# Kernel optimization log

Measured on AMD Instinct MI355X. Metric: run time of the kernel, lower is better.

## Reference

```python
import jax, jax.numpy as jnp
import numpy as np
from jax import lax

B, D, H = 16384, 64, 1024
CLAMP = 10.0


def _masks(D, H):
    # Exactly mirrors MADE.create_masks (numpy, static).
    m_in = np.arange(D)
    m0 = np.arange(H) % (D - 1)
    mask1 = (m_in[None, :] <= m0[:, None]).astype(np.float32)        # [H, D]
    base = (m0[None, :] < m_in[:, None]).astype(np.float32)          # [D, H]
    mask2 = np.repeat(base, 2, axis=0).astype(np.float32)            # [2D, H] (rows interleaved, as np.repeat)
    return jnp.asarray(mask1), jnp.asarray(mask2)


def setup_inputs() -> dict:
    key = jax.random.key(0)
    k1, k2, k3 = jax.random.split(key, 3)
    z = jax.random.normal(k1, (B, D), dtype=jnp.float32)
    xavier_std = 0.01 * np.sqrt(2.0 / (D + H))  # xavier_normal_ with gain=0.01
    W1 = jax.random.normal(k2, (H, D), dtype=jnp.float32) * xavier_std
    b1 = jnp.zeros((H,), dtype=jnp.float32)
    # original zero-inits W2 (degenerate identity flow); use small random instead
    W2 = jax.random.normal(k3, (2 * D, H), dtype=jnp.float32) * 0.01
    b2 = jnp.zeros((2 * D,), dtype=jnp.float32)
    return {"z": z, "W1": W1, "b1": b1, "W2": W2, "b2": b2}


def reference(z, W1, b1, W2, b2):
    Bd, Dd = z.shape
    Hd = W1.shape[0]
    mask1, mask2 = _masks(Dd, Hd)
    W1m = W1 * mask1
    W2m = W2 * mask2

    def conditioner(x):  # MADE.forward
        h = jnp.tanh(x @ W1m.T + b1)                 # [B, H]
        return jnp.clip(h @ W2m.T + b2, -CLAMP, CLAMP)  # [B, 2D]

    def step(carry, i):
        x, ld = carry
        params = conditioner(x)
        mu = params[:, :Dd]
        alpha = jnp.clip(params[:, Dd:], -CLAMP, CLAMP)
        a_i = alpha[:, i]                            # [B]
        x_i = z[:, i] * jnp.exp(a_i) + mu[:, i]
        x = x.at[:, i].set(x_i)
        return (x, ld + a_i), None

    init = (jnp.zeros_like(z), jnp.zeros((Bd,), dtype=z.dtype))
    (x, log_det), _ = lax.scan(step, init, jnp.arange(Dd))

    x = jnp.where(jnp.isnan(x) | jnp.isinf(x), 0.0, x)
    log_det = jnp.where(jnp.isnan(log_det) | jnp.isinf(log_det), 0.0, log_det)
    return x, log_det


if __name__ == "__main__":
    out = reference(**setup_inputs())
    print(out[0].shape, out[1].shape)
```

## Files before the change

kernel.cpp:

```cpp
#include <hip/hip_runtime.h>
#include <math.h>

#define B_DIM 16384
#define D_DIM 64
#define H_DIM 1024
#define CLAMP_V 10.0f

typedef __fp16 h2 __attribute__((ext_vector_type(2)));

__device__ __forceinline__ void inv_perm(int hp, int &c, int &h) {
    int q;
    if (hp < 272) { c = hp / 17; q = hp % 17; }
    else          { c = ((hp - 272) >> 4) + 16; q = (hp - 272) & 15; }
    h = (D_DIM - 1) * q + c;
}

__global__ __launch_bounds__(256) void maf_prep_kernel(
    const float* __restrict__ W1, const float* __restrict__ W2,
    const float* __restrict__ b1,
    __fp16* __restrict__ W1h, __fp16* __restrict__ W2h,
    __fp16* __restrict__ b1p) {
    __shared__ float smem[4224];
    __fp16* smh = reinterpret_cast<__fp16*>(smem);
    const int tid = threadIdx.x;
    const int blk = blockIdx.x;

    if (blk < 8) {
        const int hp0 = blk * 128;
        const int col = tid & 63;
        const int rr_base = tid >> 6;
        for (int rr0 = 0; rr0 < 128; rr0 += 4) {
            int rr = rr0 + rr_base;
            int c, h;
            inv_perm(hp0 + rr, c, h);
            smh[rr * 66 + col] = (__fp16)W1[h * D_DIM + col];
        }
        __syncthreads();
        const int hpt = tid & 127;
        const int ib = tid >> 7;
        int c, h;
        inv_perm(hp0 + hpt, c, h);
        for (int i0 = 0; i0 < 64; i0 += 2) {
            int i = i0 + ib;
            W1h[i * H_DIM + hp0 + hpt] =
                (i <= c) ? smh[hpt * 66 + i] : (__fp16)0.0f;
        }
    } else if (blk < 136) {
        const int j = blk - 8;
        reinterpret_cast<float4*>(smem)[tid] =
            reinterpret_cast<const float4*>(W2 + j * H_DIM)[tid];
        __syncthreads();
        const int jm = j >> 1;
#pragma unroll
        for (int kk = 0; kk < 4; kk++) {
            int hp = tid + 256 * kk;
            int c, h;
            inv_perm(hp, c, h);
            W2h[j * H_DIM + hp] = (c < jm) ? (__fp16)smem[h] : (__fp16)0.0f;
        }
    } else {
        reinterpret_cast<float4*>(smem)[tid] =
            reinterpret_cast<const float4*>(b1)[tid];
        __syncthreads();
#pragma unroll
        for (int kk = 0; kk < 4; kk++) {
            int hp = tid + 256 * kk;
            int c, h;
            inv_perm(hp, c, h);
            b1p[hp] = (__fp16)smem[h];
        }
    }
}

__device__ __forceinline__ h2 tanh_h2(h2 x) {
    h2 x2 = x * x;
    h2 p = __builtin_elementwise_fma(
        x2, h2{(__fp16)-0.33333333f, (__fp16)-0.33333333f},
        h2{(__fp16)1.0f, (__fp16)1.0f});
    return x * p;
}

__device__ __forceinline__ float clampv(float v) {
    return fminf(fmaxf(v, -CLAMP_V), CLAMP_V);
}
__device__ __forceinline__ h2 pkfma(h2 a, h2 b, h2 c) {
    return __builtin_elementwise_fma(a, b, c);
}
__device__ __forceinline__ float readlane_f(float v, int l) {
    return __int_as_float(__builtin_amdgcn_readlane(__float_as_int(v), l));
}

template<int CTRL>
__device__ __forceinline__ float dpp_add_(float v) {
    int m = __builtin_amdgcn_update_dpp(0, __float_as_int(v), CTRL, 0xf, 0xf, true);
    return v + __int_as_float(m);
}
__device__ __forceinline__ float rowsum16(float v) {
    v = dpp_add_<0x121>(v);
    v = dpp_add_<0x122>(v);
    v = dpp_add_<0x124>(v);
    v = dpp_add_<0x128>(v);
    return v;
}

__device__ __forceinline__ int stage_dst(int f) {
    int st = f / 320;
    int w  = f - st * 320;
    int base, rw;
    if (w < 64)       { base = 0;   rw = w; }
    else if (w < 192) { base = 64;  rw = w - 64; }
    else              { base = 192; rw = w - 192; }
    int c = rw >> 5, ww = rw & 31;
    return st * 320 + base + c * 32 + (ww >> 1) + ((ww & 1) << 4);
}

__device__ __forceinline__ float4 stage_ld1(int f, int gi,
        const __fp16* __restrict__ W1h, const __fp16* __restrict__ W2h) {
    int st = f / 320;
    int w  = f - st * 320;
    int i  = gi * 4 + st;
    const float4* p;
    if (w < 64)
        p = reinterpret_cast<const float4*>(W2h + i * H_DIM) + w;
    else if (w < 192)
        p = reinterpret_cast<const float4*>(W2h + (D_DIM + i) * H_DIM) + (w - 64);
    else
        p = reinterpret_cast<const float4*>(W1h + i * H_DIM) + (w - 192);
    return *p;
}

__device__ __forceinline__ void stage_load(float4 (&R)[5], int tid, int gi,
        const __fp16* __restrict__ W1h, const __fp16* __restrict__ W2h) {
#pragma unroll
    for (int kk = 0; kk < 5; kk++)
        R[kk] = stage_ld1(tid + 256 * kk, gi, W1h, W2h);
}

__device__ __forceinline__ void stage_write(float4* slabF4, float4 (&R)[5],
                                            int tid) {
#pragma unroll
    for (int kk = 0; kk < 5; kk++)
        slabF4[stage_dst(tid + 256 * kk)] = R[kk];
}

template<int MU, int AL, int UL>
__device__ __forceinline__ void lds_loadbufs(
    const float4* __restrict__ sf4, int sb, int r,
    float4 (&wm)[2 * MU], float4 (&wa)[2 * AL], float4 (&w1)[2 * (4 - UL)])
{
#pragma unroll
    for (int k = 0; k < MU; k++) {
        wm[2 * k]     = sf4[sb + k * 32 + r];
        wm[2 * k + 1] = sf4[sb + k * 32 + r + 16];
    }
#pragma unroll
    for (int k = 0; k < AL; k++) {
        wa[2 * k]     = sf4[sb + 64 + k * 32 + r];
        wa[2 * k + 1] = sf4[sb + 64 + k * 32 + r + 16];
    }
#pragma unroll
    for (int k = 0; k < 4 - UL; k++) {
        w1[2 * k]     = sf4[sb + 192 + (UL + k) * 32 + r];
        w1[2 * k + 1] = sf4[sb + 192 + (UL + k) * 32 + r + 16];
    }
}

template<int MU, int AL, int UL, int S>
__device__ __forceinline__ void do_step(
    int i, int r, const float4* __restrict__ sf4,
    float4 (&wmC)[2 * MU], float4 (&waC)[2 * AL], float4 (&w1C)[2 * (4 - UL)],
    float4 (&wmN)[2 * MU], float4 (&waN)[2 * AL], float4 (&w1N)[2 * (4 - UL)],
    float zC0, float &zN0,
    h2 (&s)[4][8], float4 &xr, float &ld,
    const float* __restrict__ zrow0,
    float b2m_v, float b2a_v)
{
    if constexpr (S < 3) {
        lds_loadbufs<MU, AL, UL>(sf4, (S + 1) * 320, r, wmN, waN, w1N);
        zN0 = zrow0[(i + 1) & 63];
    }

    const float b2mu = readlane_f(b2m_v, i);
    const float b2al = readlane_f(b2a_v, i);

    const h2 z0 = h2{(__fp16)0.0f, (__fp16)0.0f};
    h2 aM0 = z0, aM1 = z0;
    h2 aA0 = z0, aA1 = z0, aA2 = z0, aA3 = z0;
#pragma unroll
    for (int k = 0; k < AL; k++) {
        const float* wmf = reinterpret_cast<const float*>(&wmC[2 * k]);
        const float* waf = reinterpret_cast<const float*>(&waC[2 * k]);
#pragma unroll
        for (int j = 0; j < 8; j++) {
            h2 p = (k < UL) ? s[k][j] : tanh_h2(s[k][j]);
            if (k < MU) {
                if (j & 1) aM1 = pkfma(p, __builtin_bit_cast(h2, wmf[j]), aM1);
                else       aM0 = pkfma(p, __builtin_bit_cast(h2, wmf[j]), aM0);
            }
            switch (j & 3) {
                case 0: aA0 = pkfma(p, __builtin_bit_cast(h2, waf[j]), aA0); break;
                case 1: aA1 = pkfma(p, __builtin_bit_cast(h2, waf[j]), aA1); break;
                case 2: aA2 = pkfma(p, __builtin_bit_cast(h2, waf[j]), aA2); break;
                case 3: aA3 = pkfma(p, __builtin_bit_cast(h2, waf[j]), aA3); break;
            }
        }
    }
    h2 aM = aM0 + aM1;
    h2 aA = (aA0 + aA1) + (aA2 + aA3);
    float dm = rowsum16((float)aM.x + (float)aM.y);
    float da = rowsum16((float)aA.x + (float)aA.y);

    const bool mine = (r == (i >> 2));
    float mu = clampv(dm + b2mu);
    float al = clampv(da + b2al);
    float xi = fmaf(zC0, __expf(al), mu);
    ld += al;
    if (S == 0) xr.x = mine ? xi : xr.x;
    if (S == 1) xr.y = mine ? xi : xr.y;
    if (S == 2) xr.z = mine ? xi : xr.z;
    if (S == 3) xr.w = mine ? xi : xr.w;
    __fp16 xh = (__fp16)xi;
    h2 xi2 = h2{xh, xh};
#pragma unroll
    for (int k = UL; k < 4; k++) {
        const float* w1f = reinterpret_cast<const float*>(&w1C[2 * (k - UL)]);
#pragma unroll
        for (int j = 0; j < 8; j++)
            s[k][j] = pkfma(xi2, __builtin_bit_cast(h2, w1f[j]), s[k][j]);
    }
}

template<int MU, int AL, int UL, int BUF>
__device__ __forceinline__ void do_group(
    int gi, int r, int tid,
    float4 (&slab)[2][1280], float4 (&R)[5],
    h2 (&s)[4][8], float4 &xr, float &ld,
    const float* __restrict__ zrow0, float b2m_v, float b2a_v,
    const __fp16* __restrict__ W1h, const __fp16* __restrict__ W2h)
{
    stage_write(&slab[BUF][0], R, tid);
    __syncthreads();
    stage_load(R, tid, (gi + 1) & 15, W1h, W2h);
    const float4* sf4 = &slab[BUF][0];
    float4 wmA[2 * MU], waA[2 * AL], w1A[2 * (4 - UL)];
    float4 wmB[2 * MU], waB[2 * AL], w1B[2 * (4 - UL)];
    lds_loadbufs<MU, AL, UL>(sf4, 0, r, wmA, waA, w1A);
    const int i0 = gi * 4;
    float zA0 = zrow0[i0], zB0;
    do_step<MU, AL, UL, 0>(i0,     r, sf4, wmA, waA, w1A, wmB, waB, w1B,
                           zA0, zB0, s, xr, ld, zrow0, b2m_v, b2a_v);
    do_step<MU, AL, UL, 1>(i0 + 1, r, sf4, wmB, waB, w1B, wmA, waA, w1A,
                           zB0, zA0, s, xr, ld, zrow0, b2m_v, b2a_v);
    do_step<MU, AL, UL, 2>(i0 + 2, r, sf4, wmA, waA, w1A, wmB, waB, w1B,
                           zA0, zB0, s, xr, ld, zrow0, b2m_v, b2a_v);
    do_step<MU, AL, UL, 3>(i0 + 3, r, sf4, wmB, waB, w1B, wmA, waA, w1A,
                           zB0, zA0, s, xr, ld, zrow0, b2m_v, b2a_v);
}

template<int MU, int AL, int UL>
__device__ __forceinline__ void run_phase(
    int P, int r, int tid,
    float4 (&slab)[2][1280], float4 (&R)[5],
    h2 (&s)[4][8], float4 &xr, float &ld,
    const float* __restrict__ zrow0, float b2m_v, float b2a_v,
    const __fp16* __restrict__ W1h, const __fp16* __restrict__ W2h)
{
#pragma unroll 1
    for (int pp = 0; pp < 2; pp++) {
        do_group<MU, AL, UL, 0>(4 * P + 2 * pp,     r, tid, slab, R, s, xr, ld,
                                zrow0, b2m_v, b2a_v, W1h, W2h);
        do_group<MU, AL, UL, 1>(4 * P + 2 * pp + 1, r, tid, slab, R, s, xr, ld,
                                zrow0, b2m_v, b2a_v, W1h, W2h);
    }
}

__global__ __launch_bounds__(256, 1) void maf_main_kernel(
    const float* __restrict__ z, const float* __restrict__ b2,
    const __fp16* __restrict__ W1h, const __fp16* __restrict__ W2h,
    const __fp16* __restrict__ b1p, float* __restrict__ out)
{
    __shared__ float4 slab[2][1280];
    const int tid = threadIdx.x;
    const int wave = tid >> 6;
    const int lane = tid & 63;
    const int g = lane >> 4;
    const int r = lane & 15;
    const int b0 = (blockIdx.x * 4 + wave) * 4 + g;

    h2 s[4][8];
    const h2* b1p2 = reinterpret_cast<const h2*>(b1p);
#pragma unroll
    for (int c = 0; c < 4; c++) {
        int base = c * 128 + r * 8;
#pragma unroll
        for (int j = 0; j < 8; j++) s[c][j] = b1p2[base + j];
    }

    const float* zrow0 = z + b0 * D_DIM;
    const float b2m_v = b2[lane];
    const float b2a_v = b2[D_DIM + lane];
    float4 xr = float4{0, 0, 0, 0};
    float ld = 0.0f;

    float4 R[5];
    stage_load(R, tid, 0, W1h, W2h);

    run_phase<1, 3, 0>(0, r, tid, slab, R, s, xr, ld, zrow0, b2m_v, b2a_v, W1h, W2h);
#pragma unroll
    for (int j = 0; j < 8; j++) s[0][j] = tanh_h2(s[0][j]);
    run_phase<1, 3, 1>(1, r, tid, slab, R, s, xr, ld, zrow0, b2m_v, b2a_v, W1h, W2h);
#pragma unroll
    for (int j = 0; j < 8; j++) s[1][j] = tanh_h2(s[1][j]);
    run_phase<2, 4, 2>(2, r, tid, slab, R, s, xr, ld, zrow0, b2m_v, b2a_v, W1h, W2h);
#pragma unroll
    for (int j = 0; j < 8; j++) s[2][j] = tanh_h2(s[2][j]);
    run_phase<2, 4, 3>(3, r, tid, slab, R, s, xr, ld, zrow0, b2m_v, b2a_v, W1h, W2h);

    float4 v = xr;
    v.x = isfinite(v.x) ? v.x : 0.0f;
    v.y = isfinite(v.y) ? v.y : 0.0f;
    v.z = isfinite(v.z) ? v.z : 0.0f;
    v.w = isfinite(v.w) ? v.w : 0.0f;
    *reinterpret_cast<float4*>(out + b0 * D_DIM + r * 4) = v;
    if (r == 0) {
        float l = isfinite(ld) ? ld : 0.0f;
        out[B_DIM * D_DIM + b0] = l;
    }
}

extern "C" void kernel_launch(void* const* d_in, const int* in_sizes, int n_in,
                              void* d_out, int out_size, void* d_ws, size_t ws_size,
                              hipStream_t stream) {
    const float* z  = (const float*)d_in[0];
    const float* W1 = (const float*)d_in[1];
    const float* b1 = (const float*)d_in[2];
    const float* W2 = (const float*)d_in[3];
    const float* b2 = (const float*)d_in[4];
    float* out = (float*)d_out;

    __fp16* W1h = (__fp16*)d_ws;
    __fp16* W2h = W1h + D_DIM * H_DIM;
    __fp16* b1p = W2h + 2 * D_DIM * H_DIM;

    maf_prep_kernel<<<137, 256, 0, stream>>>(W1, W2, b1, W1h, W2h, b1p);

    maf_main_kernel<<<B_DIM / 16, 256, 0, stream>>>(z, b2, W1h, W2h, b1p, out);
}
```

Baseline: 165.7 us.

## Process two batch rows per lane group to reuse LDS weight loads

Each 16-lane group now carries hidden state for two batch rows instead of one, so every weight fragment read from LDS is used twice. Blocks shrink to 128 threads (2 waves), each still covering 16 rows, and the staging loop issues 10 loads per thread instead of 5. The aim is to halve LDS weight traffic per row and cut the number of block-level barriers per row. In exchange, register pressure roughly doubles for the hidden state, and with fewer waves per block there is less latency hiding.

After: 192.6 us. 1.16x slower.

```diff
diff --git a/kernel.cpp b/kernel.cpp
--- a/kernel.cpp
+++ b/kernel.cpp
@@ -129,18 +129,18 @@
     return *p;
 }
 
-__device__ __forceinline__ void stage_load(float4 (&R)[5], int tid, int gi,
+__device__ __forceinline__ void stage_load(float4 (&R)[10], int tid, int gi,
         const __fp16* __restrict__ W1h, const __fp16* __restrict__ W2h) {
 #pragma unroll
-    for (int kk = 0; kk < 5; kk++)
-        R[kk] = stage_ld1(tid + 256 * kk, gi, W1h, W2h);
-}
-
-__device__ __forceinline__ void stage_write(float4* slabF4, float4 (&R)[5],
+    for (int kk = 0; kk < 10; kk++)
+        R[kk] = stage_ld1(tid + 128 * kk, gi, W1h, W2h);
+}
+
+__device__ __forceinline__ void stage_write(float4* slabF4, float4 (&R)[10],
                                             int tid) {
 #pragma unroll
-    for (int kk = 0; kk < 5; kk++)
-        slabF4[stage_dst(tid + 256 * kk)] = R[kk];
+    for (int kk = 0; kk < 10; kk++)
+        slabF4[stage_dst(tid + 128 * kk)] = R[kk];
 }
 
 template<int MU, int AL, int UL>
@@ -170,72 +170,82 @@
     int i, int r, const float4* __restrict__ sf4,
     float4 (&wmC)[2 * MU], float4 (&waC)[2 * AL], float4 (&w1C)[2 * (4 - UL)],
     float4 (&wmN)[2 * MU], float4 (&waN)[2 * AL], float4 (&w1N)[2 * (4 - UL)],
-    float zC0, float &zN0,
-    h2 (&s)[4][8], float4 &xr, float &ld,
-    const float* __restrict__ zrow0,
+    float zC0, float zC1, float &zN0, float &zN1,
+    h2 (&s)[2][4][8], float4 (&xr)[2], float (&ld)[2],
+    const float* __restrict__ zrow0, const float* __restrict__ zrow1,
     float b2m_v, float b2a_v)
 {
     if constexpr (S < 3) {
         lds_loadbufs<MU, AL, UL>(sf4, (S + 1) * 320, r, wmN, waN, w1N);
         zN0 = zrow0[(i + 1) & 63];
+        zN1 = zrow1[(i + 1) & 63];
     }
 
     const float b2mu = readlane_f(b2m_v, i);
     const float b2al = readlane_f(b2a_v, i);
 
-    const h2 z0 = h2{(__fp16)0.0f, (__fp16)0.0f};
-    h2 aM0 = z0, aM1 = z0;
-    h2 aA0 = z0, aA1 = z0, aA2 = z0, aA3 = z0;
-#pragma unroll
-    for (int k = 0; k < AL; k++) {
-        const float* wmf = reinterpret_cast<const float*>(&wmC[2 * k]);
-        const float* waf = reinterpret_cast<const float*>(&waC[2 * k]);
-#pragma unroll
-        for (int j = 0; j < 8; j++) {
-            h2 p = (k < UL) ? s[k][j] : tanh_h2(s[k][j]);
-            if (k < MU) {
-                if (j & 1) aM1 = pkfma(p, __builtin_bit_cast(h2, wmf[j]), aM1);
-                else       aM0 = pkfma(p, __builtin_bit_cast(h2, wmf[j]), aM0);
+    float dm[2], da[2];
+#pragma unroll
+    for (int e = 0; e < 2; e++) {
+        const h2 z0 = h2{(__fp16)0.0f, (__fp16)0.0f};
+        h2 aM0 = z0, aM1 = z0;
+        h2 aA0 = z0, aA1 = z0, aA2 = z0, aA3 = z0;
+#pragma unroll
+        for (int k = 0; k < AL; k++) {
+            const float* wmf = reinterpret_cast<const float*>(&wmC[2 * k]);
+            const float* waf = reinterpret_cast<const float*>(&waC[2 * k]);
+#pragma unroll
+            for (int j = 0; j < 8; j++) {
+                h2 p = (k < UL) ? s[e][k][j] : tanh_h2(s[e][k][j]);
+                if (k < MU) {
+                    if (j & 1) aM1 = pkfma(p, __builtin_bit_cast(h2, wmf[j]), aM1);
+                    else       aM0 = pkfma(p, __builtin_bit_cast(h2, wmf[j]), aM0);
+                }
+                switch (j & 3) {
+                    case 0: aA0 = pkfma(p, __builtin_bit_cast(h2, waf[j]), aA0); break;
+                    case 1: aA1 = pkfma(p, __builtin_bit_cast(h2, waf[j]), aA1); break;
+                    case 2: aA2 = pkfma(p, __builtin_bit_cast(h2, waf[j]), aA2); break;
+                    case 3: aA3 = pkfma(p, __builtin_bit_cast(h2, waf[j]), aA3); break;
+                }
             }
-            switch (j & 3) {
-                case 0: aA0 = pkfma(p, __builtin_bit_cast(h2, waf[j]), aA0); break;
-                case 1: aA1 = pkfma(p, __builtin_bit_cast(h2, waf[j]), aA1); break;
-                case 2: aA2 = pkfma(p, __builtin_bit_cast(h2, waf[j]), aA2); break;
-                case 3: aA3 = pkfma(p, __builtin_bit_cast(h2, waf[j]), aA3); break;
-            }
-        }
-    }
-    h2 aM = aM0 + aM1;
-    h2 aA = (aA0 + aA1) + (aA2 + aA3);
-    float dm = rowsum16((float)aM.x + (float)aM.y);
-    float da = rowsum16((float)aA.x + (float)aA.y);
+        }
+        h2 aM = aM0 + aM1;
+        h2 aA = (aA0 + aA1) + (aA2 + aA3);
+        dm[e] = rowsum16((float)aM.x + (float)aM.y);
+        da[e] = rowsum16((float)aA.x + (float)aA.y);
+    }
 
     const bool mine = (r == (i >> 2));
-    float mu = clampv(dm + b2mu);
-    float al = clampv(da + b2al);
-    float xi = fmaf(zC0, __expf(al), mu);
-    ld += al;
-    if (S == 0) xr.x = mine ? xi : xr.x;
-    if (S == 1) xr.y = mine ? xi : xr.y;
-    if (S == 2) xr.z = mine ? xi : xr.z;
-    if (S == 3) xr.w = mine ? xi : xr.w;
-    __fp16 xh = (__fp16)xi;
-    h2 xi2 = h2{xh, xh};
-#pragma unroll
-    for (int k = UL; k < 4; k++) {
-        const float* w1f = reinterpret_cast<const float*>(&w1C[2 * (k - UL)]);
-#pragma unroll
-        for (int j = 0; j < 8; j++)
-            s[k][j] = pkfma(xi2, __builtin_bit_cast(h2, w1f[j]), s[k][j]);
+#pragma unroll
+    for (int e = 0; e < 2; e++) {
+        float mu = clampv(dm[e] + b2mu);
+        float al = clampv(da[e] + b2al);
+        float zi = (e == 0) ? zC0 : zC1;
+        float xi = fmaf(zi, __expf(al), mu);
+        ld[e] += al;
+        if (S == 0) xr[e].x = mine ? xi : xr[e].x;
+        if (S == 1) xr[e].y = mine ? xi : xr[e].y;
+        if (S == 2) xr[e].z = mine ? xi : xr[e].z;
+        if (S == 3) xr[e].w = mine ? xi : xr[e].w;
+        __fp16 xh = (__fp16)xi;
+        h2 xi2 = h2{xh, xh};
+#pragma unroll
+        for (int k = UL; k < 4; k++) {
+            const float* w1f = reinterpret_cast<const float*>(&w1C[2 * (k - UL)]);
+#pragma unroll
+            for (int j = 0; j < 8; j++)
+                s[e][k][j] = pkfma(xi2, __builtin_bit_cast(h2, w1f[j]), s[e][k][j]);
+        }
     }
 }
 
 template<int MU, int AL, int UL, int BUF>
 __device__ __forceinline__ void do_group(
     int gi, int r, int tid,
-    float4 (&slab)[2][1280], float4 (&R)[5],
-    h2 (&s)[4][8], float4 &xr, float &ld,
-    const float* __restrict__ zrow0, float b2m_v, float b2a_v,
+    float4 (&slab)[2][1280], float4 (&R)[10],
+    h2 (&s)[2][4][8], float4 (&xr)[2], float (&ld)[2],
+    const float* __restrict__ zrow0, const float* __restrict__ zrow1,
+    float b2m_v, float b2a_v,
     const __fp16* __restrict__ W1h, const __fp16* __restrict__ W2h)
 {
     stage_write(&slab[BUF][0], R, tid);
@@ -246,35 +256,40 @@
     float4 wmB[2 * MU], waB[2 * AL], w1B[2 * (4 - UL)];
     lds_loadbufs<MU, AL, UL>(sf4, 0, r, wmA, waA, w1A);
     const int i0 = gi * 4;
-    float zA0 = zrow0[i0], zB0;
+    float zA0 = zrow0[i0], zA1 = zrow1[i0], zB0, zB1;
     do_step<MU, AL, UL, 0>(i0,     r, sf4, wmA, waA, w1A, wmB, waB, w1B,
-                           zA0, zB0, s, xr, ld, zrow0, b2m_v, b2a_v);
+                           zA0, zA1, zB0, zB1, s, xr, ld,
+                           zrow0, zrow1, b2m_v, b2a_v);
     do_step<MU, AL, UL, 1>(i0 + 1, r, sf4, wmB, waB, w1B, wmA, waA, w1A,
-                           zB0, zA0, s, xr, ld, zrow0, b2m_v, b2a_v);
+                           zB0, zB1, zA0, zA1, s, xr, ld,
+                           zrow0, zrow1, b2m_v, b2a_v);
     do_step<MU, AL, UL, 2>(i0 + 2, r, sf4, wmA, waA, w1A, wmB, waB, w1B,
-                           zA0, zB0, s, xr, ld, zrow0, b2m_v, b2a_v);
+                           zA0, zA1, zB0, zB1, s, xr, ld,
+                           zrow0, zrow1, b2m_v, b2a_v);
     do_step<MU, AL, UL, 3>(i0 + 3, r, sf4, wmB, waB, w1B, wmA, waA, w1A,
-                           zB0, zA0, s, xr, ld, zrow0, b2m_v, b2a_v);
+                           zB0, zB1, zA0, zA1, s, xr, ld,
+                           zrow0, zrow1, b2m_v, b2a_v);
 }
 
 template<int MU, int AL, int UL>
 __device__ __forceinline__ void run_phase(
     int P, int r, int tid,
-    float4 (&slab)[2][1280], float4 (&R)[5],
-    h2 (&s)[4][8], float4 &xr, float &ld,
-    const float* __restrict__ zrow0, float b2m_v, float b2a_v,
+    float4 (&slab)[2][1280], float4 (&R)[10],
+    h2 (&s)[2][4][8], float4 (&xr)[2], float (&ld)[2],
+    const float* __restrict__ zrow0, const float* __restrict__ zrow1,
+    float b2m_v, float b2a_v,
     const __fp16* __restrict__ W1h, const __fp16* __restrict__ W2h)
 {
 #pragma unroll 1
     for (int pp = 0; pp < 2; pp++) {
         do_group<MU, AL, UL, 0>(4 * P + 2 * pp,     r, tid, slab, R, s, xr, ld,
-                                zrow0, b2m_v, b2a_v, W1h, W2h);
+                                zrow0, zrow1, b2m_v, b2a_v, W1h, W2h);
         do_group<MU, AL, UL, 1>(4 * P + 2 * pp + 1, r, tid, slab, R, s, xr, ld,
-                                zrow0, b2m_v, b2a_v, W1h, W2h);
-    }
-}
-
-__global__ __launch_bounds__(256, 1) void maf_main_kernel(
+                                zrow0, zrow1, b2m_v, b2a_v, W1h, W2h);
+    }
+}
+
+__global__ __launch_bounds__(128, 1) void maf_main_kernel(
     const float* __restrict__ z, const float* __restrict__ b2,
     const __fp16* __restrict__ W1h, const __fp16* __restrict__ W2h,
     const __fp16* __restrict__ b1p, float* __restrict__ out)
@@ -285,46 +300,67 @@
     const int lane = tid & 63;
     const int g = lane >> 4;
     const int r = lane & 15;
-    const int b0 = (blockIdx.x * 4 + wave) * 4 + g;
-
-    h2 s[4][8];
+    const int bw = (blockIdx.x * 2 + wave) * 8;
+    const int b0 = bw + g;
+    const int b1i = bw + 4 + g;
+
+    h2 s[2][4][8];
     const h2* b1p2 = reinterpret_cast<const h2*>(b1p);
 #pragma unroll
     for (int c = 0; c < 4; c++) {
         int base = c * 128 + r * 8;
 #pragma unroll
-        for (int j = 0; j < 8; j++) s[c][j] = b1p2[base + j];
+        for (int j = 0; j < 8; j++) {
+            h2 v = b1p2[base + j];
+            s[0][c][j] = v;
+            s[1][c][j] = v;
+        }
     }
 
     const float* zrow0 = z + b0 * D_DIM;
+    const float* zrow1 = z + b1i * D_DIM;
     const float b2m_v = b2[lane];
     const float b2a_v = b2[D_DIM + lane];
-    float4 xr = float4{0, 0, 0, 0};
-    float ld = 0.0f;
-
-    float4 R[5];
+    float4 xr[2] = {float4{0, 0, 0, 0}, float4{0, 0, 0, 0}};
+    float ld[2] = {0.0f, 0.0f};
+
+    float4 R[10];
     stage_load(R, tid, 0, W1h, W2h);
 
-    run_phase<1, 3, 0>(0, r, tid, slab, R, s, xr, ld, zrow0, b2m_v, b2a_v, W1h, W2h);
-#pragma unroll
-    for (int j = 0; j < 8; j++) s[0][j] = tanh_h2(s[0][j]);
-    run_phase<1, 3, 1>(1, r, tid, slab, R, s, xr, ld, zrow0, b2m_v, b2a_v, W1h, W2h);
-#pragma unroll
-    for (int j = 0; j < 8; j++) s[1][j] = tanh_h2(s[1][j]);
-    run_phase<2, 4, 2>(2, r, tid, slab, R, s, xr, ld, zrow0, b2m_v, b2a_v, W1h, W2h);
-#pragma unroll
-    for (int j = 0; j < 8; j++) s[2][j] = tanh_h2(s[2][j]);
-    run_phase<2, 4, 3>(3, r, tid, slab, R, s, xr, ld, zrow0, b2m_v, b2a_v, W1h, W2h);
-
-    float4 v = xr;
-    v.x = isfinite(v.x) ? v.x : 0.0f;
-    v.y = isfinite(v.y) ? v.y : 0.0f;
-    v.z = isfinite(v.z) ? v.z : 0.0f;
-    v.w = isfinite(v.w) ? v.w : 0.0f;
-    *reinterpret_cast<float4*>(out + b0 * D_DIM + r * 4) = v;
-    if (r == 0) {
-        float l = isfinite(ld) ? ld : 0.0f;
-        out[B_DIM * D_DIM + b0] = l;
+    run_phase<1, 3, 0>(0, r, tid, slab, R, s, xr, ld, zrow0, zrow1,
+                       b2m_v, b2a_v, W1h, W2h);
+#pragma unroll
+    for (int e = 0; e < 2; e++)
+#pragma unroll
+        for (int j = 0; j < 8; j++) s[e][0][j] = tanh_h2(s[e][0][j]);
+    run_phase<1, 3, 1>(1, r, tid, slab, R, s, xr, ld, zrow0, zrow1,
+                       b2m_v, b2a_v, W1h, W2h);
+#pragma unroll
+    for (int e = 0; e < 2; e++)
+#pragma unroll
+        for (int j = 0; j < 8; j++) s[e][1][j] = tanh_h2(s[e][1][j]);
+    run_phase<2, 4, 2>(2, r, tid, slab, R, s, xr, ld, zrow0, zrow1,
+                       b2m_v, b2a_v, W1h, W2h);
+#pragma unroll
+    for (int e = 0; e < 2; e++)
+#pragma unroll
+        for (int j = 0; j < 8; j++) s[e][2][j] = tanh_h2(s[e][2][j]);
+    run_phase<2, 4, 3>(3, r, tid, slab, R, s, xr, ld, zrow0, zrow1,
+                       b2m_v, b2a_v, W1h, W2h);
+
+#pragma unroll
+    for (int e = 0; e < 2; e++) {
+        float4 v = xr[e];
+        v.x = isfinite(v.x) ? v.x : 0.0f;
+        v.y = isfinite(v.y) ? v.y : 0.0f;
+        v.z = isfinite(v.z) ? v.z : 0.0f;
+        v.w = isfinite(v.w) ? v.w : 0.0f;
+        int b = (e == 0) ? b0 : b1i;
+        *reinterpret_cast<float4*>(out + b * D_DIM + r * 4) = v;
+        if (r == 0) {
+            float l = isfinite(ld[e]) ? ld[e] : 0.0f;
+            out[B_DIM * D_DIM + b] = l;
+        }
     }
 }
 
@@ -344,5 +380,5 @@
 
     maf_prep_kernel<<<137, 256, 0, stream>>>(W1, W2, b1, W1h, W2h, b1p);
 
-    maf_main_kernel<<<B_DIM / 16, 256, 0, stream>>>(z, b2, W1h, W2h, b1p, out);
-}
+    maf_main_kernel<<<B_DIM / 16, 128, 0, stream>>>(z, b2, W1h, W2h, b1p, out);
+}
```

## Prepack weights in LDS slab order and stream them with global_load_lds

Applied to the files above, without the earlier changes.

The prep kernel now writes W1/W2 into one packed buffer already in the per-step LDS slab layout, so each group's weight slab is one contiguous 20 KB chunk. The main kernel replaces the register-staged global load plus scattered LDS write with direct global-to-LDS DMA (global_load_lds) into the other double buffer. The aim is to drop the staging registers and the index math, and to overlap the next group's fetch with compute. The risk is ordering: the DMA writes to LDS must be complete before the following __syncthreads, and that depends on the compiler inserting the right vmcnt waits.

Measured after the change: 185.2 us. +11.8%, slower.

```diff
diff --git a/kernel.cpp b/kernel.cpp
--- a/kernel.cpp
+++ b/kernel.cpp
@@ -15,11 +15,17 @@
     h = (D_DIM - 1) * q + c;
 }
 
+__device__ __forceinline__ int reg_dst16(int hp) {
+    int f4 = hp >> 3;
+    int c4 = f4 >> 5, ww = f4 & 31;
+    int dstf4 = c4 * 32 + (ww >> 1) + ((ww & 1) << 4);
+    return dstf4 * 8 + (hp & 7);
+}
+
 __global__ __launch_bounds__(256) void maf_prep_kernel(
     const float* __restrict__ W1, const float* __restrict__ W2,
     const float* __restrict__ b1,
-    __fp16* __restrict__ W1h, __fp16* __restrict__ W2h,
-    __fp16* __restrict__ b1p) {
+    __fp16* __restrict__ Wp, __fp16* __restrict__ b1p) {
     __shared__ float smem[4224];
     __fp16* smh = reinterpret_cast<__fp16*>(smem);
     const int tid = threadIdx.x;
@@ -40,9 +46,10 @@
         const int ib = tid >> 7;
         int c, h;
         inv_perm(hp0 + hpt, c, h);
+        const int d16 = reg_dst16(hp0 + hpt);
         for (int i0 = 0; i0 < 64; i0 += 2) {
             int i = i0 + ib;
-            W1h[i * H_DIM + hp0 + hpt] =
+            Wp[i * 2560 + 1536 + d16] =
                 (i <= c) ? smh[hpt * 66 + i] : (__fp16)0.0f;
         }
     } else if (blk < 136) {
@@ -51,12 +58,24 @@
             reinterpret_cast<const float4*>(W2 + j * H_DIM)[tid];
         __syncthreads();
         const int jm = j >> 1;
-#pragma unroll
-        for (int kk = 0; kk < 4; kk++) {
-            int hp = tid + 256 * kk;
-            int c, h;
-            inv_perm(hp, c, h);
-            W2h[j * H_DIM + hp] = (c < jm) ? (__fp16)smem[h] : (__fp16)0.0f;
+        if (j < 64) {
+#pragma unroll
+            for (int kk = 0; kk < 2; kk++) {
+                int hp = tid + 256 * kk;
+                int c, h;
+                inv_perm(hp, c, h);
+                Wp[j * 2560 + reg_dst16(hp)] =
+                    (c < jm) ? (__fp16)smem[h] : (__fp16)0.0f;
+            }
+        } else {
+#pragma unroll
+            for (int kk = 0; kk < 4; kk++) {
+                int hp = tid + 256 * kk;
+                int c, h;
+                inv_perm(hp, c, h);
+                Wp[(j - 64) * 2560 + 512 + reg_dst16(hp)] =
+                    (c < jm) ? (__fp16)smem[h] : (__fp16)0.0f;
+            }
         }
     } else {
         reinterpret_cast<float4*>(smem)[tid] =
@@ -103,44 +122,20 @@
     return v;
 }
 
-__device__ __forceinline__ int stage_dst(int f) {
-    int st = f / 320;
-    int w  = f - st * 320;
-    int base, rw;
-    if (w < 64)       { base = 0;   rw = w; }
-    else if (w < 192) { base = 64;  rw = w - 64; }
-    else              { base = 192; rw = w - 192; }
-    int c = rw >> 5, ww = rw & 31;
-    return st * 320 + base + c * 32 + (ww >> 1) + ((ww & 1) << 4);
-}
-
-__device__ __forceinline__ float4 stage_ld1(int f, int gi,
-        const __fp16* __restrict__ W1h, const __fp16* __restrict__ W2h) {
-    int st = f / 320;
-    int w  = f - st * 320;
-    int i  = gi * 4 + st;
-    const float4* p;
-    if (w < 64)
-        p = reinterpret_cast<const float4*>(W2h + i * H_DIM) + w;
-    else if (w < 192)
-        p = reinterpret_cast<const float4*>(W2h + (D_DIM + i) * H_DIM) + (w - 64);
-    else
-        p = reinterpret_cast<const float4*>(W1h + i * H_DIM) + (w - 192);
-    return *p;
-}
-
-__device__ __forceinline__ void stage_load(float4 (&R)[5], int tid, int gi,
-        const __fp16* __restrict__ W1h, const __fp16* __restrict__ W2h) {
+__device__ __forceinline__ void gl_lds16(const void* g, void* l) {
+    __builtin_amdgcn_global_load_lds(
+        (const __attribute__((address_space(1))) unsigned int*)g,
+        (__attribute__((address_space(3))) unsigned int*)l,
+        16, 0, 0);
+}
+
+__device__ __forceinline__ void stage_dma(float4* dst, const float4* wp4,
+                                          int gi, int tid) {
+    const char* g = reinterpret_cast<const char*>(wp4 + gi * 1280) + tid * 16;
+    char* l = reinterpret_cast<char*>(dst) + tid * 16;
 #pragma unroll
     for (int kk = 0; kk < 5; kk++)
-        R[kk] = stage_ld1(tid + 256 * kk, gi, W1h, W2h);
-}
-
-__device__ __forceinline__ void stage_write(float4* slabF4, float4 (&R)[5],
-                                            int tid) {
-#pragma unroll
-    for (int kk = 0; kk < 5; kk++)
-        slabF4[stage_dst(tid + 256 * kk)] = R[kk];
+        gl_lds16(g + kk * 4096, l + kk * 4096);
 }
 
 template<int MU, int AL, int UL>
@@ -233,14 +228,14 @@
 template<int MU, int AL, int UL, int BUF>
 __device__ __forceinline__ void do_group(
     int gi, int r, int tid,
-    float4 (&slab)[2][1280], float4 (&R)[5],
+    float4 (&slab)[2][1280],
     h2 (&s)[4][8], float4 &xr, float &ld,
     const float* __restrict__ zrow0, float b2m_v, float b2a_v,
-    const __fp16* __restrict__ W1h, const __fp16* __restrict__ W2h)
-{
-    stage_write(&slab[BUF][0], R, tid);
+    const float4* __restrict__ wp4)
+{
     __syncthreads();
-    stage_load(R, tid, (gi + 1) & 15, W1h, W2h);
+    if (gi < 15)
+        stage_dma(&slab[BUF ^ 1][0], wp4, gi + 1, tid);
     const float4* sf4 = &slab[BUF][0];
     float4 wmA[2 * MU], waA[2 * AL], w1A[2 * (4 - UL)];
     float4 wmB[2 * MU], waB[2 * AL], w1B[2 * (4 - UL)];
@@ -260,24 +255,24 @@
 template<int MU, int AL, int UL>
 __device__ __forceinline__ void run_phase(
     int P, int r, int tid,
-    float4 (&slab)[2][1280], float4 (&R)[5],
+    float4 (&slab)[2][1280],
     h2 (&s)[4][8], float4 &xr, float &ld,
     const float* __restrict__ zrow0, float b2m_v, float b2a_v,
-    const __fp16* __restrict__ W1h, const __fp16* __restrict__ W2h)
+    const float4* __restrict__ wp4)
 {
 #pragma unroll 1
     for (int pp = 0; pp < 2; pp++) {
-        do_group<MU, AL, UL, 0>(4 * P + 2 * pp,     r, tid, slab, R, s, xr, ld,
-                                zrow0, b2m_v, b2a_v, W1h, W2h);
-        do_group<MU, AL, UL, 1>(4 * P + 2 * pp + 1, r, tid, slab, R, s, xr, ld,
-                                zrow0, b2m_v, b2a_v, W1h, W2h);
+        do_group<MU, AL, UL, 0>(4 * P + 2 * pp,     r, tid, slab, s, xr, ld,
+                                zrow0, b2m_v, b2a_v, wp4);
+        do_group<MU, AL, UL, 1>(4 * P + 2 * pp + 1, r, tid, slab, s, xr, ld,
+                                zrow0, b2m_v, b2a_v, wp4);
     }
 }
 
 __global__ __launch_bounds__(256, 1) void maf_main_kernel(
     const float* __restrict__ z, const float* __restrict__ b2,
-    const __fp16* __restrict__ W1h, const __fp16* __restrict__ W2h,
-    const __fp16* __restrict__ b1p, float* __restrict__ out)
+    const __fp16* __restrict__ Wp, const __fp16* __restrict__ b1p,
+    float* __restrict__ out)
 {
     __shared__ float4 slab[2][1280];
     const int tid = threadIdx.x;
@@ -286,6 +281,9 @@
     const int g = lane >> 4;
     const int r = lane & 15;
     const int b0 = (blockIdx.x * 4 + wave) * 4 + g;
+    const float4* wp4 = reinterpret_cast<const float4*>(Wp);
+
+    stage_dma(&slab[0][0], wp4, 0, tid);
 
     h2 s[4][8];
     const h2* b1p2 = reinterpret_cast<const h2*>(b1p);
@@ -302,19 +300,16 @@
     float4 xr = float4{0, 0, 0, 0};
     float ld = 0.0f;
 
-    float4 R[5];
-    stage_load(R, tid, 0, W1h, W2h);
-
-    run_phase<1, 3, 0>(0, r, tid, slab, R, s, xr, ld, zrow0, b2m_v, b2a_v, W1h, W2h);
+    run_phase<1, 3, 0>(0, r, tid, slab, s, xr, ld, zrow0, b2m_v, b2a_v, wp4);
 #pragma unroll
     for (int j = 0; j < 8; j++) s[0][j] = tanh_h2(s[0][j]);
-    run_phase<1, 3, 1>(1, r, tid, slab, R, s, xr, ld, zrow0, b2m_v, b2a_v, W1h, W2h);
+    run_phase<1, 3, 1>(1, r, tid, slab, s, xr, ld, zrow0, b2m_v, b2a_v, wp4);
 #pragma unroll
     for (int j = 0; j < 8; j++) s[1][j] = tanh_h2(s[1][j]);
-    run_phase<2, 4, 2>(2, r, tid, slab, R, s, xr, ld, zrow0, b2m_v, b2a_v, W1h, W2h);
+    run_phase<2, 4, 2>(2, r, tid, slab, s, xr, ld, zrow0, b2m_v, b2a_v, wp4);
 #pragma unroll
     for (int j = 0; j < 8; j++) s[2][j] = tanh_h2(s[2][j]);
-    run_phase<2, 4, 3>(3, r, tid, slab, R, s, xr, ld, zrow0, b2m_v, b2a_v, W1h, W2h);
+    run_phase<2, 4, 3>(3, r, tid, slab, s, xr, ld, zrow0, b2m_v, b2a_v, wp4);
 
     float4 v = xr;
     v.x = isfinite(v.x) ? v.x : 0.0f;
@@ -338,11 +333,10 @@
     const float* b2 = (const float*)d_in[4];
     float* out = (float*)d_out;
 
-    __fp16* W1h = (__fp16*)d_ws;
-    __fp16* W2h = W1h + D_DIM * H_DIM;
-    __fp16* b1p = W2h + 2 * D_DIM * H_DIM;
-
-    maf_prep_kernel<<<137, 256, 0, stream>>>(W1, W2, b1, W1h, W2h, b1p);
-
-    maf_main_kernel<<<B_DIM / 16, 256, 0, stream>>>(z, b2, W1h, W2h, b1p, out);
-}
+    __fp16* Wp  = (__fp16*)d_ws;
+    __fp16* b1p = Wp + 64 * 2560;
+
+    maf_prep_kernel<<<137, 256, 0, stream>>>(W1, W2, b1, Wp, b1p);
+
+    maf_main_kernel<<<B_DIM / 16, 256, 0, stream>>>(z, b2, Wp, b1p, out);
+}
```
